# Kernel tuning notes

Measured on AMD Instinct MI355X. Metric: run time of the kernel, lower is better.

Reference implementation:

```python
import jax, jax.numpy as jnp
import numpy as np

N = 100000   # nodes
E = 600000   # edges
IN = 12      # in_dim
H = 128      # hidden_dim
OUT = 2      # out_dim
L = 3        # num_layers
EPS = 1e-5   # BatchNorm eps


def setup_inputs() -> dict:
    key = jax.random.key(0)
    ks = jax.random.split(key, 14)
    s = 0.05
    return {
        "features": jax.random.normal(ks[0], (N, IN), jnp.float32),
        "edge_index": jax.random.randint(ks[1], (2, E), 0, N, dtype=jnp.int32).astype(jnp.int64),
        "emb_W": jax.random.normal(ks[2], (IN, H), jnp.float32) * s,
        "emb_b": jnp.zeros((H,), jnp.float32),
        "Wself": jax.random.normal(ks[3], (L, H, H), jnp.float32) * s,
        "Wneigh": jax.random.normal(ks[4], (L, H, H), jnp.float32) * s,
        "conv_b": jnp.zeros((L, H), jnp.float32),
        "bn_gamma": jnp.ones((L, H), jnp.float32),
        "bn_beta": jnp.zeros((L, H), jnp.float32),
        "W1": jax.random.normal(ks[5], (H, H // 2), jnp.float32) * s,
        "b1": jnp.zeros((H // 2,), jnp.float32),
        "W2": jax.random.normal(ks[6], (H // 2, OUT), jnp.float32) * s,
        "b2": jnp.zeros((OUT,), jnp.float32),
    }


def reference(features, edge_index, emb_W, emb_b, Wself, Wneigh, conv_b,
              bn_gamma, bn_beta, W1, b1, W2, b2):
    src, dst = edge_index[0], edge_index[1]
    # in-degree per destination node (loop-invariant)
    deg = jax.ops.segment_sum(jnp.ones((E,), features.dtype), dst, num_segments=N)
    inv_deg = 1.0 / jnp.maximum(deg, 1.0)  # [N]

    h = features @ emb_W + emb_b           # embedding: [N, H]
    h_last = h
    for i in range(L):
        # SAGEConv 'mean': gather src feats, scatter-sum to dst, divide by degree
        msg_sum = jax.ops.segment_sum(h[src], dst, num_segments=N)  # [N, H]
        h_neigh = msg_sum * inv_deg[:, None]
        h_new = h @ Wself[i] + h_neigh @ Wneigh[i] + conv_b[i]
        # BatchNorm1d over nodes (batch statistics)
        mu = jnp.mean(h_new, axis=0)
        var = jnp.var(h_new, axis=0)
        h_new = (h_new - mu) * jax.lax.rsqrt(var + EPS) * bn_gamma[i] + bn_beta[i]
        h_new = jax.nn.relu(h_new)
        # dropout is identity at inference
        if i > 0:
            h_new = h_new + h_last  # residual
        h_last = h_new
        h = h_new
    # MLP head
    out = jax.nn.relu(h @ W1 + b1) @ W2 + b2  # [N, 2]
    return out
```

## Files before the change

kernel.cpp:

```cpp
#include <hip/hip_runtime.h>
#include <hip/hip_bf16.h>
#include <cstdint>

#define H 128
#define EPS 1e-5f
#define CAP 32
#define NB 16

typedef unsigned int uint;
typedef unsigned short ushort;
typedef short short8 __attribute__((ext_vector_type(8)));
typedef float f32x4 __attribute__((ext_vector_type(4)));

__device__ __forceinline__ ushort f2bf(float f) {
  uint u = __float_as_uint(f);
  u += 0x7fffu + ((u >> 16) & 1u);
  return (ushort)(u >> 16);
}
__device__ __forceinline__ float bflo(uint v) { return __uint_as_float(v << 16); }
__device__ __forceinline__ float bfhi(uint v) { return __uint_as_float(v & 0xffff0000u); }
__device__ __forceinline__ float nrm(float x, float sc, float sh) {
  return fmaxf(fmaf(x, sc, sh), 0.f);
}

__global__ __launch_bounds__(256) void k_zero(const void* __restrict__ ei, int N,
                                              uint* __restrict__ cnt, int* __restrict__ flag,
                                              float* __restrict__ bn_all,
                                              ushort* __restrict__ bufA, ushort* __restrict__ bufB) {
  int b = blockIdx.x, t = threadIdx.x;
  int i = b * 256 + t;
  if (i < N) cnt[i] = 0u;
  if (b == 0) {
    for (int j = t; j < NB * 256 * 3; j += 256) bn_all[j] = 0.f;
    if (t < 128) {
      bufA[(size_t)N * H + t] = 0;
      bufB[(size_t)N * H + t] = 0;
    }
    if (t == 0) {
      const long long* p = (const long long*)ei;
      int ok = 1;
      for (int j = 0; j < 16; ++j) {
        long long s = p[j];
        if (s < 0 || s >= (long long)N) ok = 0;
      }
      *flag = ok;
    }
  }
}

__global__ __launch_bounds__(256) void k_work(const void* __restrict__ ei, uint* __restrict__ cnt,
                                              uint* __restrict__ csr, int E, const int* __restrict__ flag,
                                              const float* __restrict__ F, const float* __restrict__ embW,
                                              const float* __restrict__ embB, ushort* __restrict__ bufA,
                                              const float* __restrict__ Wself, const float* __restrict__ Wneigh,
                                              const float* __restrict__ W1,
                                              ushort* __restrict__ Wsw, ushort* __restrict__ W1sw,
                                              int N, int FB, int EB) {
  __shared__ float sW[12 * 128];
  __shared__ float sF[256 * 12];
  int b = blockIdx.x, t = threadIdx.x;
  if (b < FB) {
    int e0 = (b * 256 + t) * 2;
    if (e0 >= E) return;
    int is64 = *flag;
    int s0, s1 = -1, d0, d1 = -1;
    bool two = (e0 + 1 < E);
    if (is64) {
      const unsigned long long* p = (const unsigned long long*)ei;
      if (two) {
        ulong2 sv = *(const ulong2*)(p + e0);
        ulong2 dv = *(const ulong2*)(p + E + e0);
        s0 = (int)sv.x; s1 = (int)sv.y; d0 = (int)dv.x; d1 = (int)dv.y;
      } else {
        s0 = (int)p[e0]; d0 = (int)p[E + e0];
      }
    } else {
      const int* p = (const int*)ei;
      if (two) {
        int2 sv = *(const int2*)(p + e0);
        int2 dv = *(const int2*)(p + E + e0);
        s0 = sv.x; s1 = sv.y; d0 = dv.x; d1 = dv.y;
      } else {
        s0 = p[e0]; d0 = p[E + e0];
      }
    }
    uint p0 = atomicAdd(&cnt[d0], 1u);
    if (p0 < (uint)CAP) csr[(size_t)d0 * CAP + p0] = (uint)s0;
    if (two) {
      uint p1 = atomicAdd(&cnt[d1], 1u);
      if (p1 < (uint)CAP) csr[(size_t)d1 * CAP + p1] = (uint)s1;
    }
    return;
  }
  if (b < FB + EB) {
    int blk = b - FB;
    for (int i = t; i < 12 * 128; i += 256) sW[i] = embW[i];
    int row0 = blk * 256;
    int nrows = min(256, N - row0);
    for (int i = t; i < nrows * 12; i += 256) sF[i] = F[(size_t)row0 * 12 + i];
    __syncthreads();
    int col = t & 127, half = t >> 7;
    float bias = embB[col];
    int rlo = half * 128, rhi = min(nrows, rlo + 128);
    for (int r = rlo; r < rhi; ++r) {
      float acc = bias;
#pragma unroll
      for (int k = 0; k < 12; ++k) acc = fmaf(sF[r * 12 + k], sW[k * 128 + col], acc);
      bufA[(size_t)(row0 + r) * H + col] = f2bf(acc);
    }
    return;
  }
  int e = (b - FB - EB) * 256 + t;
  if (e < 3 * 4096) {
    int l = e >> 12, r = e & 4095;
    int kt = r >> 9, nt = (r >> 6) & 7, lane = r & 63;
    int quad = lane >> 4, l16 = lane & 15;
    int n = nt * 16 + l16;
    ushort* dst = Wsw + ((size_t)l * 4096 + (kt * 8 + nt) * 64 + lane) * 8;
#pragma unroll
    for (int j = 0; j < 8; ++j) {
      int k = kt * 32 + quad * 8 + j;
      float v = (k < 128) ? Wself[(size_t)l * H * H + (size_t)k * H + n]
                          : Wneigh[(size_t)l * H * H + (size_t)(k - 128) * H + n];
      dst[j] = f2bf(v);
    }
  } else if (e < 3 * 4096 + 1024) {
    int r = e - 3 * 4096;
    int kt = r >> 8, nt = (r >> 6) & 3, lane = r & 63;
    int quad = lane >> 4, l16 = lane & 15;
    int n = nt * 16 + l16;
    ushort* dst = W1sw + ((size_t)((kt * 4 + nt) * 64 + lane)) * 8;
#pragma unroll
    for (int j = 0; j < 8; ++j) {
      int k = kt * 32 + quad * 8 + j;
      dst[j] = f2bf(W1[(size_t)k * 64 + n]);
    }
  }
}

__global__ __launch_bounds__(256, 4) void k_gg(const ushort* __restrict__ h, ushort* __restrict__ z,
                                               const uint* __restrict__ cnt, const uint* __restrict__ csr,
                                               const ushort* __restrict__ Wsw, const float* __restrict__ bias,
                                               float* __restrict__ bn_acc, int N) {
  __shared__ ushort sMsg[128 * 128];
  int tid = threadIdx.x;
  int wave = tid >> 6, lane = tid & 63, quad = lane >> 4, l16 = lane & 15;
  int row0 = blockIdx.x * 128;
  int wrow0 = row0 + wave * 32;
  short8 zf8 = {0, 0, 0, 0, 0, 0, 0, 0};

  short8 aS[4][2];
#pragma unroll
  for (int kt = 0; kt < 4; ++kt) {
    int colb = kt * 32 + quad * 8;
#pragma unroll
    for (int m = 0; m < 2; ++m) {
      int row = wrow0 + m * 16 + l16;
      aS[kt][m] = (row < N) ? *(const short8*)(h + (size_t)row * H + colb) : zf8;
    }
  }

  {
    const uint4* hu = (const uint4*)h;
#pragma unroll
    for (int p = 0; p < 8; ++p) {
      int nl = p * 16 + wave * 4 + quad;
      int n = row0 + nl;
      uint rawc = (n < N) ? cnt[n] : 0u;
      uint deg = min(rawc, (uint)CAP);
      const uint* row = csr + (size_t)n * CAP;
      float a0 = 0.f, a1 = 0.f, a2 = 0.f, a3 = 0.f, a4 = 0.f, a5 = 0.f, a6 = 0.f, a7 = 0.f;
      for (uint k = 0; k < deg; k += 8) {
        uint4 r0 = *(const uint4*)(row + k);
        uint4 r1 = *(const uint4*)(row + k + 4);
        uint raw[8] = {r0.x, r0.y, r0.z, r0.w, r1.x, r1.y, r1.z, r1.w};
        uint idx[8];
#pragma unroll
        for (int j = 0; j < 8; ++j) idx[j] = (k + j < deg) ? raw[j] : (uint)N;
        uint4 v[8];
#pragma unroll
        for (int j = 0; j < 8; ++j) v[j] = hu[(size_t)idx[j] * 16 + l16];
#pragma unroll
        for (int j = 0; j < 8; ++j) {
          a0 += bflo(v[j].x); a1 += bfhi(v[j].x);
          a2 += bflo(v[j].y); a3 += bfhi(v[j].y);
          a4 += bflo(v[j].z); a5 += bfhi(v[j].z);
          a6 += bflo(v[j].w); a7 += bfhi(v[j].w);
        }
      }
      float inv = 1.0f / (float)max(rawc, 1u);
      uint4 o;
      o.x = (uint)f2bf(a0 * inv) | ((uint)f2bf(a1 * inv) << 16);
      o.y = (uint)f2bf(a2 * inv) | ((uint)f2bf(a3 * inv) << 16);
      o.z = (uint)f2bf(a4 * inv) | ((uint)f2bf(a5 * inv) << 16);
      o.w = (uint)f2bf(a6 * inv) | ((uint)f2bf(a7 * inv) << 16);
      int off = nl * 256 + ((l16 * 16) ^ ((nl & 7) << 4));
      *(uint4*)((char*)sMsg + off) = o;
    }
  }

  f32x4 acc[2][8];
#pragma unroll
  for (int m = 0; m < 2; ++m)
#pragma unroll
    for (int nt = 0; nt < 8; ++nt) acc[m][nt] = (f32x4){0.f, 0.f, 0.f, 0.f};
  const short8* Bp = (const short8*)Wsw;

#pragma unroll
  for (int kt = 0; kt < 4; ++kt) {
#pragma unroll
    for (int nt = 0; nt < 8; ++nt) {
      short8 bfr = Bp[(kt * 8 + nt) * 64 + lane];
#pragma unroll
      for (int m = 0; m < 2; ++m)
        acc[m][nt] = __builtin_amdgcn_mfma_f32_16x16x32_bf16(aS[kt][m], bfr, acc[m][nt], 0, 0, 0);
    }
  }
  __syncthreads();
#pragma unroll
  for (int kt = 4; kt < 8; ++kt) {
    int cb = (kt - 4) * 64 + quad * 16;
    short8 a[2];
#pragma unroll
    for (int m = 0; m < 2; ++m) {
      int rl = wave * 32 + m * 16 + l16;
      a[m] = *(const short8*)((const char*)sMsg + rl * 256 + (cb ^ ((l16 & 7) << 4)));
    }
#pragma unroll
    for (int nt = 0; nt < 8; ++nt) {
      short8 bfr = Bp[(kt * 8 + nt) * 64 + lane];
#pragma unroll
      for (int m = 0; m < 2; ++m)
        acc[m][nt] = __builtin_amdgcn_mfma_f32_16x16x32_bf16(a[m], bfr, acc[m][nt], 0, 0, 0);
    }
  }

  float bs[8];
#pragma unroll
  for (int nt = 0; nt < 8; ++nt) bs[nt] = bias[nt * 16 + l16];
  float ps[8], pq[8];
#pragma unroll
  for (int nt = 0; nt < 8; ++nt) { ps[nt] = 0.f; pq[nt] = 0.f; }
#pragma unroll
  for (int m = 0; m < 2; ++m) {
#pragma unroll
    for (int nt = 0; nt < 8; ++nt) {
      int col = nt * 16 + l16;
#pragma unroll
      for (int r = 0; r < 4; ++r) {
        int row = wrow0 + m * 16 + quad * 4 + r;
        if (row < N) {
          float v = acc[m][nt][r] + bs[nt];
          z[(size_t)row * H + col] = f2bf(v);
          ps[nt] += v; pq[nt] += v * v;
        }
      }
    }
  }
  __syncthreads();
  float* red = (float*)sMsg;
  int wq = wave * 4 + quad;
#pragma unroll
  for (int nt = 0; nt < 8; ++nt) {
    red[(wq * 8 + nt) * 17 + l16] = ps[nt];
    red[2176 + (wq * 8 + nt) * 17 + l16] = pq[nt];
  }
  __syncthreads();
  if (tid < 128) {
    int nt = tid >> 4, lc = tid & 15;
    float s = 0.f, q = 0.f;
#pragma unroll
    for (int w2i = 0; w2i < 16; ++w2i) {
      s += red[(w2i * 8 + nt) * 17 + lc];
      q += red[2176 + (w2i * 8 + nt) * 17 + lc];
    }
    float* bank = bn_acc + (size_t)(blockIdx.x & (NB - 1)) * 256;
    atomicAdd(&bank[tid], s);
    atomicAdd(&bank[128 + tid], q);
  }
}

__global__ __launch_bounds__(256) void k_norm(uint4* __restrict__ z, const uint4* __restrict__ hprev,
                                              const float* __restrict__ bn_acc,
                                              const float* __restrict__ gamma,
                                              const float* __restrict__ beta,
                                              int residual, int n4, float invN) {
  __shared__ float ssc[128], ssh[128];
  int t = threadIdx.x;
  if (t < 128) {
    float s = 0.f, q = 0.f;
#pragma unroll
    for (int b = 0; b < NB; ++b) {
      s += bn_acc[b * 256 + t];
      q += bn_acc[b * 256 + 128 + t];
    }
    float mu = s * invN;
    float var = fmaxf(q * invN - mu * mu, 0.f);
    float sc = gamma[t] * rsqrtf(var + EPS);
    ssc[t] = sc;
    ssh[t] = beta[t] - mu * sc;
  }
  __syncthreads();
  int idx = blockIdx.x * 256 + t;
  if (idx >= n4) return;
  int j = (idx & 15) * 8;
  uint4 v = z[idx];
  float x0 = nrm(bflo(v.x), ssc[j + 0], ssh[j + 0]);
  float x1 = nrm(bfhi(v.x), ssc[j + 1], ssh[j + 1]);
  float x2 = nrm(bflo(v.y), ssc[j + 2], ssh[j + 2]);
  float x3 = nrm(bfhi(v.y), ssc[j + 3], ssh[j + 3]);
  float x4 = nrm(bflo(v.z), ssc[j + 4], ssh[j + 4]);
  float x5 = nrm(bfhi(v.z), ssc[j + 5], ssh[j + 5]);
  float x6 = nrm(bflo(v.w), ssc[j + 6], ssh[j + 6]);
  float x7 = nrm(bfhi(v.w), ssc[j + 7], ssh[j + 7]);
  if (residual) {
    uint4 r = hprev[idx];
    x0 += bflo(r.x); x1 += bfhi(r.x); x2 += bflo(r.y); x3 += bfhi(r.y);
    x4 += bflo(r.z); x5 += bfhi(r.z); x6 += bflo(r.w); x7 += bfhi(r.w);
  }
  uint4 o;
  o.x = (uint)f2bf(x0) | ((uint)f2bf(x1) << 16);
  o.y = (uint)f2bf(x2) | ((uint)f2bf(x3) << 16);
  o.z = (uint)f2bf(x4) | ((uint)f2bf(x5) << 16);
  o.w = (uint)f2bf(x6) | ((uint)f2bf(x7) << 16);
  z[idx] = o;
}

__global__ __launch_bounds__(256) void k_head(const ushort* __restrict__ z, const ushort* __restrict__ hprev,
                                              const float* __restrict__ bn_acc,
                                              const float* __restrict__ gamma,
                                              const float* __restrict__ beta, float invN,
                                              const ushort* __restrict__ W1sw,
                                              const float* __restrict__ b1, const float* __restrict__ W2,
                                              const float* __restrict__ b2, float* __restrict__ out, int N) {
  __shared__ float ssc[128], ssh[128];
  int tid = threadIdx.x;
  if (tid < 128) {
    float s = 0.f, q = 0.f;
#pragma unroll
    for (int b = 0; b < NB; ++b) {
      s += bn_acc[b * 256 + tid];
      q += bn_acc[b * 256 + 128 + tid];
    }
    float mu = s * invN;
    float var = fmaxf(q * invN - mu * mu, 0.f);
    float sc = gamma[tid] * rsqrtf(var + EPS);
    ssc[tid] = sc;
    ssh[tid] = beta[tid] - mu * sc;
  }
  __syncthreads();
  int wave = tid >> 6, lane = tid & 63, quad = lane >> 4, l16 = lane & 15;
  int wrow0 = blockIdx.x * 64 + wave * 16;
  int am = wrow0 + l16;
  bool avalid = am < N;
  short8 af[4];
#pragma unroll
  for (int kt = 0; kt < 4; ++kt) {
    int c0 = kt * 32 + quad * 8;
    uint4 vz = avalid ? ((const uint4*)z)[(size_t)am * 16 + kt * 4 + quad] : make_uint4(0, 0, 0, 0);
    uint4 vr = avalid ? ((const uint4*)hprev)[(size_t)am * 16 + kt * 4 + quad] : make_uint4(0, 0, 0, 0);
    float x0 = nrm(bflo(vz.x), ssc[c0 + 0], ssh[c0 + 0]) + bflo(vr.x);
    float x1 = nrm(bfhi(vz.x), ssc[c0 + 1], ssh[c0 + 1]) + bfhi(vr.x);
    float x2 = nrm(bflo(vz.y), ssc[c0 + 2], ssh[c0 + 2]) + bflo(vr.y);
    float x3 = nrm(bfhi(vz.y), ssc[c0 + 3], ssh[c0 + 3]) + bfhi(vr.y);
    float x4 = nrm(bflo(vz.z), ssc[c0 + 4], ssh[c0 + 4]) + bflo(vr.z);
    float x5 = nrm(bfhi(vz.z), ssc[c0 + 5], ssh[c0 + 5]) + bfhi(vr.z);
    float x6 = nrm(bflo(vz.w), ssc[c0 + 6], ssh[c0 + 6]) + bflo(vr.w);
    float x7 = nrm(bfhi(vz.w), ssc[c0 + 7], ssh[c0 + 7]) + bfhi(vr.w);
    ushort u[8] = {f2bf(x0), f2bf(x1), f2bf(x2), f2bf(x3), f2bf(x4), f2bf(x5), f2bf(x6), f2bf(x7)};
    af[kt] = *(short8*)u;
  }
  const short8* Bp = (const short8*)W1sw;
  f32x4 acc[4];
#pragma unroll
  for (int nt = 0; nt < 4; ++nt) acc[nt] = (f32x4){0.f, 0.f, 0.f, 0.f};
#pragma unroll
  for (int kt = 0; kt < 4; ++kt) {
#pragma unroll
    for (int nt = 0; nt < 4; ++nt) {
      short8 bfr = Bp[(kt * 4 + nt) * 64 + lane];
      acc[nt] = __builtin_amdgcn_mfma_f32_16x16x32_bf16(af[kt], bfr, acc[nt], 0, 0, 0);
    }
  }
  float p0[4] = {0.f, 0.f, 0.f, 0.f}, p1[4] = {0.f, 0.f, 0.f, 0.f};
#pragma unroll
  for (int nt = 0; nt < 4; ++nt) {
    int c = nt * 16 + l16;
    float bc = b1[c], w20 = W2[c * 2], w21 = W2[c * 2 + 1];
#pragma unroll
    for (int r = 0; r < 4; ++r) {
      float v = fmaxf(acc[nt][r] + bc, 0.f);
      p0[r] = fmaf(v, w20, p0[r]);
      p1[r] = fmaf(v, w21, p1[r]);
    }
  }
#pragma unroll
  for (int m = 1; m < 16; m <<= 1) {
#pragma unroll
    for (int r = 0; r < 4; ++r) {
      p0[r] += __shfl_xor(p0[r], m);
      p1[r] += __shfl_xor(p1[r], m);
    }
  }
  if (l16 == 0) {
    float b20 = b2[0], b21 = b2[1];
#pragma unroll
    for (int r = 0; r < 4; ++r) {
      int row = wrow0 + quad * 4 + r;
      if (row < N) {
        float2 o = make_float2(p0[r] + b20, p1[r] + b21);
        *(float2*)(out + (size_t)row * 2) = o;
      }
    }
  }
}

extern "C" void kernel_launch(void* const* d_in, const int* in_sizes, int n_in,
                              void* d_out, int out_size, void* d_ws, size_t ws_size,
                              hipStream_t stream) {
  const float* features = (const float*)d_in[0];
  const void*  edges    = d_in[1];
  const float* emb_W    = (const float*)d_in[2];
  const float* emb_b    = (const float*)d_in[3];
  const float* Wself    = (const float*)d_in[4];
  const float* Wneigh   = (const float*)d_in[5];
  const float* conv_b   = (const float*)d_in[6];
  const float* bn_gamma = (const float*)d_in[7];
  const float* bn_beta  = (const float*)d_in[8];
  const float* W1       = (const float*)d_in[9];
  const float* b1       = (const float*)d_in[10];
  const float* W2       = (const float*)d_in[11];
  const float* b2       = (const float*)d_in[12];
  float* out = (float*)d_out;
  const int N = in_sizes[0] / 12;
  const int E = in_sizes[1] / 2;
  const float invN = 1.0f / (float)N;

  char* ws = (char*)d_ws;
  size_t off = 0;
  auto take = [&](size_t bytes) {
    char* p = ws + off;
    off = (off + bytes + 511) & ~(size_t)511;
    return p;
  };
  int*    flag   = (int*)take(4);
  uint*   cnt    = (uint*)take((size_t)N * 4);
  uint*   csr    = (uint*)take((size_t)N * CAP * 4);
  float*  bn_all = (float*)take(NB * 256 * 3 * 4);
  ushort* Wsw    = (ushort*)take(3 * 4096 * 8 * 2);
  ushort* W1sw   = (ushort*)take(1024 * 8 * 2);
  ushort* bufA   = (ushort*)take(((size_t)N + 1) * H * 2);
  ushort* bufB   = (ushort*)take(((size_t)N + 1) * H * 2);

  const int ZB = (N + 255) / 256;
  const int EB = (N + 255) / 256;
  const int PB = (3 * 4096 + 1024 + 255) / 256;
  const int FB = (E + 511) / 512;
  const int GB = (N + 127) / 128;

  k_zero<<<ZB, 256, 0, stream>>>(edges, N, cnt, flag, bn_all, bufA, bufB);
  k_work<<<FB + EB + PB, 256, 0, stream>>>(edges, cnt, csr, E, flag, features, emb_W, emb_b,
                                           bufA, Wself, Wneigh, W1, Wsw, W1sw, N, FB, EB);

  ushort* hbuf = bufA;
  ushort* obuf = bufB;
  const int n4 = N * 16;
  for (int i = 0; i < 3; ++i) {
    float* bn_i = bn_all + (size_t)i * NB * 256;
    k_gg<<<GB, 256, 0, stream>>>(hbuf, obuf, cnt, csr, Wsw + (size_t)i * 4096 * 8,
                                 conv_b + (size_t)i * H, bn_i, N);
    if (i < 2) {
      k_norm<<<(n4 + 255) / 256, 256, 0, stream>>>((uint4*)obuf, (const uint4*)hbuf, bn_i,
                                                   bn_gamma + (size_t)i * H, bn_beta + (size_t)i * H,
                                                   (i > 0) ? 1 : 0, n4, invN);
      ushort* t = hbuf; hbuf = obuf; obuf = t;
    }
  }
  k_head<<<(N + 63) / 64, 256, 0, stream>>>(obuf, hbuf, bn_all + (size_t)2 * NB * 256,
                                            bn_gamma + 2 * H, bn_beta + 2 * H,
                                            invN, W1sw, b1, W2, b2, out, N);
}
```

Before: 311.1 us.

## Aggregate raw 12-dim features for layer 0 using precomposed embedding-neighbor weights

Layer 0 now gathers and averages the 12-wide bf16 input features instead of the 128-wide embedded rows. The neighbor term is computed as mean(F)·(embW·Wneigh) plus a degree-indicator times (embB·Wneigh), using weights precomposed in the init kernel. This cuts the layer-0 gather traffic roughly eightfold and replaces four MFMA k-steps with a small scalar FMA loop. The zero/embed kernels are merged and CSR fill is split into its own launch. The cost is extra precompute, different rounding (bf16 features in place of bf16 embeddings), and scalar FMA work inside the GEMM kernel.

Result: slower. 571.6 us (+83.7%).

```diff
diff --git a/kernel.cpp b/kernel.cpp
--- a/kernel.cpp
+++ b/kernel.cpp
@@ -23,77 +23,40 @@
   return fmaxf(fmaf(x, sc, sh), 0.f);
 }
 
-__global__ __launch_bounds__(256) void k_zero(const void* __restrict__ ei, int N,
+__global__ __launch_bounds__(256) void k_init(const void* __restrict__ ei, int N,
                                               uint* __restrict__ cnt, int* __restrict__ flag,
-                                              float* __restrict__ bn_all,
-                                              ushort* __restrict__ bufA, ushort* __restrict__ bufB) {
-  int b = blockIdx.x, t = threadIdx.x;
-  int i = b * 256 + t;
-  if (i < N) cnt[i] = 0u;
-  if (b == 0) {
-    for (int j = t; j < NB * 256 * 3; j += 256) bn_all[j] = 0.f;
-    if (t < 128) {
-      bufA[(size_t)N * H + t] = 0;
-      bufB[(size_t)N * H + t] = 0;
-    }
-    if (t == 0) {
-      const long long* p = (const long long*)ei;
-      int ok = 1;
-      for (int j = 0; j < 16; ++j) {
-        long long s = p[j];
-        if (s < 0 || s >= (long long)N) ok = 0;
-      }
-      *flag = ok;
-    }
-  }
-}
-
-__global__ __launch_bounds__(256) void k_work(const void* __restrict__ ei, uint* __restrict__ cnt,
-                                              uint* __restrict__ csr, int E, const int* __restrict__ flag,
                                               const float* __restrict__ F, const float* __restrict__ embW,
-                                              const float* __restrict__ embB, ushort* __restrict__ bufA,
+                                              const float* __restrict__ embB,
+                                              ushort* __restrict__ bufA, ushort* __restrict__ bufB,
                                               const float* __restrict__ Wself, const float* __restrict__ Wneigh,
                                               const float* __restrict__ W1,
                                               ushort* __restrict__ Wsw, ushort* __restrict__ W1sw,
-                                              int N, int FB, int EB) {
+                                              float* __restrict__ bn_all,
+                                              ushort* __restrict__ Fbf, float* __restrict__ Wp,
+                                              float* __restrict__ bp,
+                                              int ZB, int EB) {
   __shared__ float sW[12 * 128];
   __shared__ float sF[256 * 12];
   int b = blockIdx.x, t = threadIdx.x;
-  if (b < FB) {
-    int e0 = (b * 256 + t) * 2;
-    if (e0 >= E) return;
-    int is64 = *flag;
-    int s0, s1 = -1, d0, d1 = -1;
-    bool two = (e0 + 1 < E);
-    if (is64) {
-      const unsigned long long* p = (const unsigned long long*)ei;
-      if (two) {
-        ulong2 sv = *(const ulong2*)(p + e0);
-        ulong2 dv = *(const ulong2*)(p + E + e0);
-        s0 = (int)sv.x; s1 = (int)sv.y; d0 = (int)dv.x; d1 = (int)dv.y;
-      } else {
-        s0 = (int)p[e0]; d0 = (int)p[E + e0];
-      }
-    } else {
-      const int* p = (const int*)ei;
-      if (two) {
-        int2 sv = *(const int2*)(p + e0);
-        int2 dv = *(const int2*)(p + E + e0);
-        s0 = sv.x; s1 = sv.y; d0 = dv.x; d1 = dv.y;
-      } else {
-        s0 = p[e0]; d0 = p[E + e0];
-      }
-    }
-    uint p0 = atomicAdd(&cnt[d0], 1u);
-    if (p0 < (uint)CAP) csr[(size_t)d0 * CAP + p0] = (uint)s0;
-    if (two) {
-      uint p1 = atomicAdd(&cnt[d1], 1u);
-      if (p1 < (uint)CAP) csr[(size_t)d1 * CAP + p1] = (uint)s1;
+  if (b < ZB) {
+    int i = b * 256 + t;
+    if (i < N) cnt[i] = 0u;
+    if (b == 0) {
+      for (int j = t; j < NB * 256 * 3; j += 256) bn_all[j] = 0.f;
+      if (t == 0) {
+        const long long* p = (const long long*)ei;
+        int ok = 1;
+        for (int j = 0; j < 16; ++j) {
+          long long s = p[j];
+          if (s < 0 || s >= (long long)N) ok = 0;
+        }
+        *flag = ok;
+      }
     }
     return;
   }
-  if (b < FB + EB) {
-    int blk = b - FB;
+  if (b < ZB + EB) {
+    int blk = b - ZB;
     for (int i = t; i < 12 * 128; i += 256) sW[i] = embW[i];
     int row0 = blk * 256;
     int nrows = min(256, N - row0);
@@ -108,9 +71,18 @@
       for (int k = 0; k < 12; ++k) acc = fmaf(sF[r * 12 + k], sW[k * 128 + col], acc);
       bufA[(size_t)(row0 + r) * H + col] = f2bf(acc);
     }
+    for (int i = t; i < nrows * 16; i += 256) {
+      int r = i >> 4, k = i & 15;
+      Fbf[(size_t)(row0 + r) * 16 + k] = (k < 12) ? f2bf(sF[r * 12 + k]) : (ushort)0;
+    }
+    if (blk == 0 && t < 128) {
+      bufA[(size_t)N * H + t] = 0;
+      bufB[(size_t)N * H + t] = 0;
+      if (t < 16) Fbf[(size_t)N * 16 + t] = 0;
+    }
     return;
   }
-  int e = (b - FB - EB) * 256 + t;
+  int e = (b - ZB - EB) * 256 + t;
   if (e < 3 * 4096) {
     int l = e >> 12, r = e & 4095;
     int kt = r >> 9, nt = (r >> 6) & 7, lane = r & 63;
@@ -135,32 +107,106 @@
       int k = kt * 32 + quad * 8 + j;
       dst[j] = f2bf(W1[(size_t)k * 64 + n]);
     }
-  }
-}
-
+  } else if (e < 3 * 4096 + 1024 + 1536) {
+    int e2 = e - (3 * 4096 + 1024);
+    int k = e2 >> 7, c = e2 & 127;
+    float acc = 0.f;
+    for (int j = 0; j < 128; ++j)
+      acc = fmaf(embW[k * 128 + j], Wneigh[(size_t)j * 128 + c], acc);
+    Wp[k * 128 + c] = acc;
+  } else if (e < 3 * 4096 + 1024 + 1664) {
+    int c = e - (3 * 4096 + 1024 + 1536);
+    float acc = 0.f;
+    for (int j = 0; j < 128; ++j)
+      acc = fmaf(embB[j], Wneigh[(size_t)j * 128 + c], acc);
+    bp[c] = acc;
+  }
+}
+
+__global__ __launch_bounds__(256) void k_fill(const void* __restrict__ ei, uint* __restrict__ cnt,
+                                              uint* __restrict__ csr, int E,
+                                              const int* __restrict__ flag) {
+  int e0 = (blockIdx.x * 256 + threadIdx.x) * 2;
+  if (e0 >= E) return;
+  int is64 = *flag;
+  int s0, s1 = -1, d0, d1 = -1;
+  bool two = (e0 + 1 < E);
+  if (is64) {
+    const unsigned long long* p = (const unsigned long long*)ei;
+    if (two) {
+      ulong2 sv = *(const ulong2*)(p + e0);
+      ulong2 dv = *(const ulong2*)(p + E + e0);
+      s0 = (int)sv.x; s1 = (int)sv.y; d0 = (int)dv.x; d1 = (int)dv.y;
+    } else {
+      s0 = (int)p[e0]; d0 = (int)p[E + e0];
+    }
+  } else {
+    const int* p = (const int*)ei;
+    if (two) {
+      int2 sv = *(const int2*)(p + e0);
+      int2 dv = *(const int2*)(p + E + e0);
+      s0 = sv.x; s1 = sv.y; d0 = dv.x; d1 = dv.y;
+    } else {
+      s0 = p[e0]; d0 = p[E + e0];
+    }
+  }
+  uint p0 = atomicAdd(&cnt[d0], 1u);
+  if (p0 < (uint)CAP) csr[(size_t)d0 * CAP + p0] = (uint)s0;
+  if (two) {
+    uint p1 = atomicAdd(&cnt[d1], 1u);
+    if (p1 < (uint)CAP) csr[(size_t)d1 * CAP + p1] = (uint)s1;
+  }
+}
+
+template <int L0>
 __global__ __launch_bounds__(256, 4) void k_gg(const ushort* __restrict__ h, ushort* __restrict__ z,
                                                const uint* __restrict__ cnt, const uint* __restrict__ csr,
                                                const ushort* __restrict__ Wsw, const float* __restrict__ bias,
-                                               float* __restrict__ bn_acc, int N) {
+                                               float* __restrict__ bn_acc, int N,
+                                               const ushort* __restrict__ Fbf, const float* __restrict__ Wp,
+                                               const float* __restrict__ bp) {
   __shared__ ushort sMsg[128 * 128];
+  __shared__ float sEW[L0 ? 1664 : 1];
   int tid = threadIdx.x;
   int wave = tid >> 6, lane = tid & 63, quad = lane >> 4, l16 = lane & 15;
   int row0 = blockIdx.x * 128;
-  int wrow0 = row0 + wave * 32;
-  short8 zf8 = {0, 0, 0, 0, 0, 0, 0, 0};
-
-  short8 aS[4][2];
-#pragma unroll
-  for (int kt = 0; kt < 4; ++kt) {
-    int colb = kt * 32 + quad * 8;
-#pragma unroll
-    for (int m = 0; m < 2; ++m) {
-      int row = wrow0 + m * 16 + l16;
-      aS[kt][m] = (row < N) ? *(const short8*)(h + (size_t)row * H + colb) : zf8;
-    }
-  }
-
-  {
+
+  if (L0) {
+    int half = lane & 1;
+    int nl = wave * 32 + (lane >> 1);
+    int n = row0 + nl;
+    uint rawc = (n < N) ? cnt[n] : 0u;
+    uint deg = min(rawc, (uint)CAP);
+    const uint* row = csr + (size_t)n * CAP;
+    const uint4* fu = (const uint4*)Fbf;
+    float a0 = 0.f, a1 = 0.f, a2 = 0.f, a3 = 0.f, a4 = 0.f, a5 = 0.f, a6 = 0.f, a7 = 0.f;
+    for (uint k = 0; k < deg; k += 8) {
+      uint4 r0 = *(const uint4*)(row + k);
+      uint4 r1 = *(const uint4*)(row + k + 4);
+      uint raw[8] = {r0.x, r0.y, r0.z, r0.w, r1.x, r1.y, r1.z, r1.w};
+      uint idx[8];
+#pragma unroll
+      for (int j = 0; j < 8; ++j) idx[j] = (k + j < deg) ? raw[j] : (uint)N;
+      uint4 v[8];
+#pragma unroll
+      for (int j = 0; j < 8; ++j) v[j] = fu[(size_t)idx[j] * 2 + half];
+#pragma unroll
+      for (int j = 0; j < 8; ++j) {
+        a0 += bflo(v[j].x); a1 += bfhi(v[j].x);
+        a2 += bflo(v[j].y); a3 += bfhi(v[j].y);
+        a4 += bflo(v[j].z); a5 += bfhi(v[j].z);
+        a6 += bflo(v[j].w); a7 += bfhi(v[j].w);
+      }
+    }
+    float inv = 1.0f / (float)max(rawc, 1u);
+    a0 *= inv; a1 *= inv; a2 *= inv; a3 *= inv;
+    a4 *= inv; a5 *= inv; a6 *= inv; a7 *= inv;
+    if (half) a4 = (rawc > 0) ? 1.f : 0.f;
+    float* fm = (float*)((char*)sMsg + nl * 256 + (((nl >> 2) & 3) << 6)) + half * 8;
+    ((f32x4*)fm)[0] = (f32x4){a0, a1, a2, a3};
+    ((f32x4*)fm)[1] = (f32x4){a4, a5, a6, a7};
+    for (int i = tid; i < 1664; i += 256) sEW[i] = (i < 1536) ? Wp[i] : bp[i - 1536];
+  } else {
     const uint4* hu = (const uint4*)h;
 #pragma unroll
     for (int p = 0; p < 8; ++p) {
@@ -199,39 +245,80 @@
     }
   }
 
+  int wrow0 = row0 + wave * 32;
   f32x4 acc[2][8];
 #pragma unroll
   for (int m = 0; m < 2; ++m)
 #pragma unroll
     for (int nt = 0; nt < 8; ++nt) acc[m][nt] = (f32x4){0.f, 0.f, 0.f, 0.f};
+  short8 zf8 = {0, 0, 0, 0, 0, 0, 0, 0};
   const short8* Bp = (const short8*)Wsw;
 
 #pragma unroll
   for (int kt = 0; kt < 4; ++kt) {
+    int colb = kt * 32 + quad * 8;
+    short8 a[2];
+#pragma unroll
+    for (int m = 0; m < 2; ++m) {
+      int row = wrow0 + m * 16 + l16;
+      a[m] = (row < N) ? *(const short8*)(h + (size_t)row * H + colb) : zf8;
+    }
 #pragma unroll
     for (int nt = 0; nt < 8; ++nt) {
       short8 bfr = Bp[(kt * 8 + nt) * 64 + lane];
 #pragma unroll
       for (int m = 0; m < 2; ++m)
-        acc[m][nt] = __builtin_amdgcn_mfma_f32_16x16x32_bf16(aS[kt][m], bfr, acc[m][nt], 0, 0, 0);
+        acc[m][nt] = __builtin_amdgcn_mfma_f32_16x16x32_bf16(a[m], bfr, acc[m][nt], 0, 0, 0);
     }
   }
   __syncthreads();
-#pragma unroll
-  for (int kt = 4; kt < 8; ++kt) {
-    int cb = (kt - 4) * 64 + quad * 16;
-    short8 a[2];
-#pragma unroll
-    for (int m = 0; m < 2; ++m) {
-      int rl = wave * 32 + m * 16 + l16;
-      a[m] = *(const short8*)((const char*)sMsg + rl * 256 + (cb ^ ((l16 & 7) << 4)));
-    }
-#pragma unroll
-    for (int nt = 0; nt < 8; ++nt) {
-      short8 bfr = Bp[(kt * 8 + nt) * 64 + lane];
-#pragma unroll
-      for (int m = 0; m < 2; ++m)
-        acc[m][nt] = __builtin_amdgcn_mfma_f32_16x16x32_bf16(a[m], bfr, acc[m][nt], 0, 0, 0);
+
+  if (L0) {
+#pragma unroll
+    for (int g = 0; g < 4; ++g) {
+      float w0[12], w1[12], wb0, wb1;
+      int c0 = (g * 2) * 16 + l16, c1 = (g * 2 + 1) * 16 + l16;
+      wb0 = sEW[1536 + c0]; wb1 = sEW[1536 + c1];
+#pragma unroll
+      for (int k = 0; k < 12; ++k) { w0[k] = sEW[k * 128 + c0]; w1[k] = sEW[k * 128 + c1]; }
+#pragma unroll
+      for (int m = 0; m < 2; ++m) {
+#pragma unroll
+        for (int r = 0; r < 4; ++r) {
+          int rl = wave * 32 + m * 16 + quad * 4 + r;
+          const float* fm = (const float*)((const char*)sMsg + rl * 256 + (((rl >> 2) & 3) << 6));
+          float fk[12];
+#pragma unroll
+          for (int k = 0; k < 12; ++k) fk[k] = fm[k];
+          float bf = fm[12];
+          float s0 = bf * wb0, s1 = bf * wb1;
+#pragma unroll
+          for (int k = 0; k < 12; ++k) {
+            s0 = fmaf(fk[k], w0[k], s0);
+            s1 = fmaf(fk[k], w1[k], s1);
+          }
+          acc[m][g * 2][r] += s0;
+          acc[m][g * 2 + 1][r] += s1;
+        }
+      }
+    }
+  } else {
+#pragma unroll
+    for (int kt = 4; kt < 8; ++kt) {
+      int cb = (kt - 4) * 64 + quad * 16;
+      short8 a[2];
+#pragma unroll
+      for (int m = 0; m < 2; ++m) {
+        int rl = wave * 32 + m * 16 + l16;
+        a[m] = *(const short8*)((const char*)sMsg + rl * 256 + (cb ^ ((l16 & 7) << 4)));
+      }
+#pragma unroll
+      for (int nt = 0; nt < 8; ++nt) {
+        short8 bfr = Bp[(kt * 8 + nt) * 64 + lane];
+#pragma unroll
+        for (int m = 0; m < 2; ++m)
+          acc[m][nt] = __builtin_amdgcn_mfma_f32_16x16x32_bf16(a[m], bfr, acc[m][nt], 0, 0, 0);
+      }
     }
   }
 
@@ -449,34 +536,37 @@
   float*  bn_all = (float*)take(NB * 256 * 3 * 4);
   ushort* Wsw    = (ushort*)take(3 * 4096 * 8 * 2);
   ushort* W1sw   = (ushort*)take(1024 * 8 * 2);
+  ushort* Fbf    = (ushort*)take(((size_t)N + 1) * 16 * 2);
+  float*  Wp     = (float*)take(1536 * 4);
+  float*  bp     = (float*)take(128 * 4);
   ushort* bufA   = (ushort*)take(((size_t)N + 1) * H * 2);
   ushort* bufB   = (ushort*)take(((size_t)N + 1) * H * 2);
 
   const int ZB = (N + 255) / 256;
   const int EB = (N + 255) / 256;
-  const int PB = (3 * 4096 + 1024 + 255) / 256;
+  const int PB = (3 * 4096 + 1024 + 1664 + 255) / 256;
   const int FB = (E + 511) / 512;
   const int GB = (N + 127) / 128;
 
-  k_zero<<<ZB, 256, 0, stream>>>(edges, N, cnt, flag, bn_all, bufA, bufB);
-  k_work<<<FB + EB + PB, 256, 0, stream>>>(edges, cnt, csr, E, flag, features, emb_W, emb_b,
-                                           bufA, Wself, Wneigh, W1, Wsw, W1sw, N, FB, EB);
-
-  ushort* hbuf = bufA;
-  ushort* obuf = bufB;
+  float* bn0 = bn_all;
+  float* bn1 = bn_all + (size_t)NB * 256;
+  float* bn2 = bn_all + (size_t)2 * NB * 256;
   const int n4 = N * 16;
-  for (int i = 0; i < 3; ++i) {
-    float* bn_i = bn_all + (size_t)i * NB * 256;
-    k_gg<<<GB, 256, 0, stream>>>(hbuf, obuf, cnt, csr, Wsw + (size_t)i * 4096 * 8,
-                                 conv_b + (size_t)i * H, bn_i, N);
-    if (i < 2) {
-      k_norm<<<(n4 + 255) / 256, 256, 0, stream>>>((uint4*)obuf, (const uint4*)hbuf, bn_i,
-                                                   bn_gamma + (size_t)i * H, bn_beta + (size_t)i * H,
-                                                   (i > 0) ? 1 : 0, n4, invN);
-      ushort* t = hbuf; hbuf = obuf; obuf = t;
-    }
-  }
-  k_head<<<(N + 63) / 64, 256, 0, stream>>>(obuf, hbuf, bn_all + (size_t)2 * NB * 256,
-                                            bn_gamma + 2 * H, bn_beta + 2 * H,
+
+  k_init<<<ZB + EB + PB, 256, 0, stream>>>(edges, N, cnt, flag, features, emb_W, emb_b,
+                                           bufA, bufB, Wself, Wneigh, W1, Wsw, W1sw, bn_all,
+                                           Fbf, Wp, bp, ZB, EB);
+  k_fill<<<FB, 256, 0, stream>>>(edges, cnt, csr, E, flag);
+
+  k_gg<1><<<GB, 256, 0, stream>>>(bufA, bufB, cnt, csr, Wsw, conv_b, bn0, N, Fbf, Wp, bp);
+  k_norm<<<(n4 + 255) / 256, 256, 0, stream>>>((uint4*)bufB, nullptr, bn0,
+                                               bn_gamma, bn_beta, 0, n4, invN);
+  k_gg<0><<<GB, 256, 0, stream>>>(bufB, bufA, cnt, csr, Wsw + (size_t)4096 * 8,
+                                  conv_b + H, bn1, N, nullptr, nullptr, nullptr);
+  k_norm<<<(n4 + 255) / 256, 256, 0, stream>>>((uint4*)bufA, (const uint4*)bufB, bn1,
+                                               bn_gamma + H, bn_beta + H, 1, n4, invN);
+  k_gg<0><<<GB, 256, 0, stream>>>(bufA, bufB, cnt, csr, Wsw + (size_t)2 * 4096 * 8,
+                                  conv_b + 2 * H, bn2, N, nullptr, nullptr, nullptr);
+  k_head<<<(N + 63) / 64, 256, 0, stream>>>(bufB, bufA, bn2, bn_gamma + 2 * H, bn_beta + 2 * H,
                                             invN, W1sw, b1, W2, b2, out, N);
 }
```
